# Optimization experiments

Measured on AMD Instinct MI355X. Metric: run time of the kernel, lower is better.

The kernel has to match this reference:

```python
import math
import jax, jax.numpy as jnp
import numpy as np

N = 8192; DEG = 32; E = N * DEG; H = 128
NB_NODE = 3; NB_EDGE = 4
UPPER_T = 1.0; LOWER_T = 0.01; NUM_ITERS = 1000
EPS_LN = 1e-5

def from_binary(s):
    # [..., bits] 0/1 ints -> integer code
    return (s * (2 ** jnp.arange(s.shape[-1], dtype=s.dtype))).sum(-1)

def layer_norm(x, g, b):
    mu = x.mean(-1, keepdims=True)
    v = ((x - mu) ** 2).mean(-1, keepdims=True)
    return (x - mu) / jnp.sqrt(v + EPS_LN) * g + b

def entmax15(logits):
    z = -jnp.sort(-logits, axis=-1)  # descending
    cz = jnp.cumsum(z, -1); cz2 = jnp.cumsum(z * z, -1)
    k = jnp.arange(1, logits.shape[-1] + 1, dtype=logits.dtype)
    mz = cz / k; mz2 = cz2 / k
    discr = jax.nn.relu(mz ** 2 - mz2 + 1.0 / k)
    tau_c = mz - jnp.sqrt(discr + 1e-8)
    kidx = (z > tau_c).sum(-1, keepdims=True)
    tau = jnp.take_along_axis(tau_c, kidx - 1, axis=-1)
    return jax.nn.relu(logits - tau) ** 2

def sparsemax(logits):
    z = -jnp.sort(-logits, axis=-1)
    cz = jnp.cumsum(z, -1)
    k = jnp.arange(1, logits.shape[-1] + 1, dtype=logits.dtype)
    kidx = (k * z > cz - 1.0).sum(-1, keepdims=True)
    cumk = jnp.take_along_axis(cz, kidx - 1, axis=-1)
    tau = (cumk - 1.0) / kidx.astype(logits.dtype)
    return jax.nn.relu(logits - tau)

def interpolated_probs(logits, u):
    p_soft = jax.nn.softmax(logits, -1)
    p15 = entmax15(logits)
    ps = sparsemax(logits)
    w_low = u * 2.0
    low = (1.0 - w_low) * p_soft + w_low * p15
    w_high = (u - 0.5) * 2.0
    high = (1.0 - w_high) * p15 + w_high * ps
    return jnp.where(u <= 0.5, low, high)

def setup_inputs():
    key = jax.random.key(0)
    ks = jax.random.split(key, 20)
    s = 1.0 / math.sqrt(H)
    node_states = jax.random.randint(ks[0], (N, NB_NODE), 0, 2, dtype=jnp.int32)
    edge_states = jax.random.randint(ks[1], (E, NB_EDGE), 0, 2, dtype=jnp.int32)
    scalars = jax.random.uniform(ks[2], (E, 1), jnp.float32)
    # uniform in-degree DEG, dst sorted, first edge per node is its self-loop
    dst = jnp.repeat(jnp.arange(N, dtype=jnp.int32), DEG)
    src = jax.random.randint(ks[3], (N, DEG), 0, N, dtype=jnp.int32).at[:, 0].set(jnp.arange(N, dtype=jnp.int32)).reshape(-1)
    edge_index = jnp.stack([src, dst])
    rev_idx = jax.random.permutation(ks[4], E).astype(jnp.int32)
    def w(k, shape):
        return jax.random.normal(k, shape, jnp.float32) * s
    return {
        'node_states': node_states, 'edge_states': edge_states, 'scalars': scalars,
        'edge_index': edge_index, 'rev_idx': rev_idx, 'training_step': 500,
        'emb_virtual': w(ks[5], (2 ** (NB_NODE + 1), H)),
        'emb_recv': w(ks[6], (2 ** (NB_NODE + 1), H)),
        'emb_edge': w(ks[7], (2 ** NB_EDGE, H)),
        'emb_static': w(ks[8], (4, H)),
        'Wq': w(ks[9], (H, H)), 'Wk': w(ks[10], (H, H)), 'Wv': w(ks[11], (H, H)),
        'Wek': w(ks[12], (H, H)), 'Wev': w(ks[13], (H, H)), 'Wcomb': w(ks[14], (3 * H, H)),
        'gW1': w(ks[15], (H, H)), 'gb1': jnp.zeros((H,), jnp.float32),
        'gW2': w(ks[16], (H, 1)), 'gb2': jnp.full((1,), -5.0, jnp.float32),
        'ln_q_s': jnp.ones((H,), jnp.float32), 'ln_q_b': jnp.zeros((H,), jnp.float32),
        'ln_k_s': jnp.ones((H,), jnp.float32), 'ln_k_b': jnp.zeros((H,), jnp.float32),
        'ln_ke_s': jnp.ones((H,), jnp.float32), 'ln_ke_b': jnp.zeros((H,), jnp.float32),
    }

def reference(node_states, edge_states, scalars, edge_index, rev_idx, training_step,
              emb_virtual, emb_recv, emb_edge, emb_static,
              Wq, Wk, Wv, Wek, Wev, Wcomb, gW1, gb1, gW2, gb2,
              ln_q_s, ln_q_b, ln_k_s, ln_k_b, ln_ke_s, ln_ke_b):
    src, dst = edge_index[0], edge_index[1]
    node_fts = emb_virtual[2 * from_binary(node_states)]   # [N,H] (use_select_best=False path)
    edge_fts = emb_edge[from_binary(edge_states)]           # [E,H]
    Q = layer_norm(node_fts @ Wq, ln_q_s, ln_q_b)
    Kn = layer_norm(node_fts @ Wk, ln_k_s, ln_k_b)
    Vn = node_fts @ Wv
    u = jax.nn.sigmoid(jax.nn.relu(node_fts @ gW1 + gb1) @ gW2 + gb2)  # [N,1] sparsity gate
    # ---- combined edge K/V ----
    sel = emb_recv[2 * from_binary(node_states[src])]
    # per-node scalars come from the unique self-loop edge of each node
    node_scalars = jnp.zeros((N, 1), scalars.dtype).at[dst].add(jnp.where((src == dst)[:, None], scalars, 0.0))
    sender_s, recv_s = node_scalars[src], node_scalars[dst]
    rlx = (scalars < recv_s).astype(jnp.int32)
    rlx_d = (sender_s + scalars < recv_s).astype(jnp.int32)
    static_fts = emb_static[from_binary(jnp.concatenate([rlx, rlx_d], -1))]
    combined = jnp.concatenate([edge_fts, edge_fts[rev_idx], static_fts], -1) @ Wcomb
    edge_K = layer_norm(sel @ Wek, ln_ke_s, ln_ke_b)
    edge_V = combined @ Wev
    Kc = Kn[src] + edge_K
    Vc = Vn[src] + edge_V
    # ---- to_dense_batch over destination node (dst is sorted) ----
    counts = jax.ops.segment_sum(jnp.ones(E, jnp.int32), dst, num_segments=N)
    starts = jnp.cumsum(counts) - counts
    pos = jnp.arange(E, dtype=jnp.int32) - starts[dst]
    denseK = jnp.zeros((N, DEG, H), Kc.dtype).at[dst, pos].set(Kc)
    denseV = jnp.zeros((N, DEG, H), Vc.dtype).at[dst, pos].set(Vc)
    mask = jnp.zeros((N, DEG), bool).at[dst, pos].set(True)
    cK = jnp.concatenate([Kn[:, None], denseK], 1)   # [N,1+DEG,H] self + neighbors
    cV = jnp.concatenate([Vn[:, None], denseV], 1)
    cmask = jnp.concatenate([jnp.ones((N, 1), bool), mask], 1)
    logits = jnp.einsum('nh,nkh->nk', Q, cK) / math.sqrt(H)
    logits = jnp.where(cmask, logits, -1e9)
    sparse_probs = interpolated_probs(logits, u)
    is_sel = (sparse_probs > 1e-4).astype(logits.dtype)
    hard = is_sel / (is_sel.sum(1, keepdims=True) + 1e-9)  # attention='entmax_average'
    if training_step == -1:
        attn = hard
    else:
        tau = UPPER_T * (LOWER_T / UPPER_T) ** (training_step / NUM_ITERS)  # temp anneal
        beta = min(max(tau, 0.01), 1.0)
        if beta > 0.01:
            sp = jax.nn.softmax(logits, -1) * cmask
            sp = sp / (sp.sum(1, keepdims=True) + 1e-9)
            gp = (1.0 - beta) * sparse_probs + beta * sp
        else:
            gp = sparse_probs
        attn = jax.lax.stop_gradient(hard - gp) + gp  # straight-through
    attn = attn * cmask
    agg = jnp.einsum('nk,nkh->nh', attn, cV)
    return node_fts + agg, edge_fts + agg[dst]
```

## Files before the change

kernel.cpp:

```cpp
#include <hip/hip_runtime.h>
#include <hip/hip_bf16.h>

#define NN 8192
#define EE 262144
#define HH 128
#define DEGC 32

#define WS_NF    0
#define WS_EF    1024
#define WS_VNT   3072
#define WS_AP    4096
#define WS_BP    6144
#define WS_CP    8192
#define WS_QT    8704
#define WS_KNT   9728
#define WS_EKT   10752
#define WS_U8    11776
#define WS_CN    11784
#define WS_NS    19976
#define WS_CE    28168
#define WS_COEF  290312

__global__ __launch_bounds__(128) void k_pre(
    const float* __restrict__ embV, const float* __restrict__ embR,
    const float* __restrict__ embE, const float* __restrict__ embS,
    const float* __restrict__ Wq, const float* __restrict__ Wk, const float* __restrict__ Wv,
    const float* __restrict__ Wev, const float* __restrict__ Wcomb,
    const float* __restrict__ gW1, const float* __restrict__ gb1,
    const float* __restrict__ gW2, const float* __restrict__ gb2,
    const float* __restrict__ Wek,
    const float* __restrict__ lnqs, const float* __restrict__ lnqb,
    const float* __restrict__ lnks, const float* __restrict__ lnkb,
    const float* __restrict__ lnes, const float* __restrict__ lneb,
    const int* __restrict__ node_states, const int* __restrict__ edge_states,
    const float* __restrict__ scalars, const int* __restrict__ src,
    float* __restrict__ ws)
{
  __shared__ float x[HH];
  __shared__ float y[HH];
  __shared__ float red[4];
  const int b = blockIdx.x, t = threadIdx.x;

  if (b < 24) {
    const int which = b >> 3, rr = b & 7;
    const float* xs = (which == 2 ? embR : embV) + 2*rr*HH;
    const float* W  = (which == 0 ? Wq : (which == 1 ? Wk : Wek));
    const float* ls = (which == 0 ? lnqs : (which == 1 ? lnks : lnes));
    const float* lb = (which == 0 ? lnqb : (which == 1 ? lnkb : lneb));
    float* outp = ws + (which == 0 ? WS_QT : (which == 1 ? WS_KNT : WS_EKT)) + rr*HH;
    x[t] = xs[t];
    __syncthreads();
    float acc = 0.f;
    for (int k = 0; k < HH; ++k) acc = fmaf(x[k], W[k*HH + t], acc);
    float s1 = acc;
    for (int off = 32; off; off >>= 1) s1 += __shfl_down(s1, off);
    if ((t & 63) == 0) red[t >> 6] = s1;
    __syncthreads();
    const float mu = (red[0] + red[1]) / 128.f;
    __syncthreads();
    const float dd = acc - mu;
    float s2 = dd * dd;
    for (int off = 32; off; off >>= 1) s2 += __shfl_down(s2, off);
    if ((t & 63) == 0) red[t >> 6] = s2;
    __syncthreads();
    const float var = (red[0] + red[1]) / 128.f;
    outp[t] = dd * (1.0f / sqrtf(var + 1e-5f)) * ls[t] + lb[t];
  } else if (b < 76) {
    int c, mode; const float* xs; const float* W1; float* outp = nullptr;
    if (b < 32)      { c = b-24; xs = embV + 2*c*HH; W1 = Wv;            mode = 0; outp = ws+WS_VNT+c*HH; }
    else if (b < 40) { c = b-32; xs = embV + 2*c*HH; W1 = gW1;           mode = 1; }
    else if (b < 56) { c = b-40; xs = embE + c*HH;   W1 = Wcomb;         mode = 2; outp = ws+WS_AP+c*HH; }
    else if (b < 72) { c = b-56; xs = embE + c*HH;   W1 = Wcomb+HH*HH;   mode = 2; outp = ws+WS_BP+c*HH; }
    else             { c = b-72; xs = embS + c*HH;   W1 = Wcomb+2*HH*HH; mode = 2; outp = ws+WS_CP+c*HH; }
    x[t] = xs[t];
    if (b >= 24 && b < 32) ws[WS_NF + c*HH + t] = x[t];
    if (b >= 40 && b < 56) ws[WS_EF + c*HH + t] = x[t];
    __syncthreads();
    float acc = 0.f;
    for (int k = 0; k < HH; ++k) acc = fmaf(x[k], W1[k*HH + t], acc);
    if (mode == 1) {
      acc = fmaxf(acc + gb1[t], 0.f);
      y[t] = acc;
      __syncthreads();
      if (t == 0) {
        float s = 0.f;
        for (int i = 0; i < HH; ++i) s += y[i] * gW2[i];
        s += gb2[0];
        ws[WS_U8 + c] = 1.0f / (1.0f + expf(-s));
      }
    } else if (mode == 2) {
      y[t] = acc;
      __syncthreads();
      float a2 = 0.f;
      for (int k = 0; k < HH; ++k) a2 = fmaf(y[k], Wev[k*HH + t], a2);
      outp[t] = a2;
    } else {
      outp[t] = acc;
    }
  } else if (b < 2124) {
    const int e = (b - 76)*128 + t;
    const int4 p = ((const int4*)edge_states)[e];
    ((int*)(ws + WS_CE))[e] = p.x + 2*p.y + 4*p.z + 8*p.w;
  } else {
    const int n = (b - 2124)*128 + t;
    const int* p = node_states + 3*n;
    ((int*)(ws + WS_CN))[n] = p[0] + 2*p[1] + 4*p[2];
    float s = 0.f;
    const int base = n*DEGC;
    for (int d = 0; d < DEGC; ++d)
      if (src[base + d] == n) s += scalars[base + d];
    ws[WS_NS + n] = s;
  }
}

__global__ __launch_bounds__(256) void k_attn(
    const int* __restrict__ src, const int* __restrict__ rev,
    const float* __restrict__ scalars, const float* __restrict__ wsf,
    const int* __restrict__ cn, const float* __restrict__ nsc,
    const int* __restrict__ ce, float* __restrict__ coef)
{
  const int t = threadIdx.x;
  const int l = t & 63;
  const int n = blockIdx.x*4 + (t >> 6);
  const int cn_n = cn[n];
  const float rs = nsc[n];
  const int base = n*DEGC;

  int cs = 0, m = 0, mr = 0; float scl = 0.f, ssv = 0.f;
  if (l < DEGC) {
    const int e = base + l;
    const int s = src[e];
    m   = ce[e];
    const int re = rev[e];
    mr  = ce[re];
    scl = scalars[e];
    cs  = cn[s];
    ssv = nsc[s];
  }

  const float invs = 0.08838834764831845f;
  const int j8 = l & 7, p8 = l >> 3;
  float part = 0.f;
  {
    const float* q  = wsf + WS_QT  + cn_n*HH;
    const float* kn = wsf + WS_KNT + j8*HH;
    const float* ek = wsf + WS_EKT + j8*HH;
    #pragma unroll
    for (int hh = 0; hh < 16; ++hh) {
      const int h = p8*16 + hh;
      part = fmaf(q[h], kn[h] + ek[h], part);
    }
  }
  part += __shfl_xor(part, 8);
  part += __shfl_xor(part, 16);
  part += __shfl_xor(part, 32);
  const float Dj = part * invs;
  float Drow[8];
  #pragma unroll
  for (int jj = 0; jj < 8; ++jj) Drow[jj] = __shfl(Dj, jj);
  float d0p;
  {
    const float* q  = wsf + WS_QT  + cn_n*HH;
    const float* kn = wsf + WS_KNT + cn_n*HH;
    d0p = q[l]*kn[l] + q[l+64]*kn[l+64];
  }
  #pragma unroll
  for (int off = 32; off; off >>= 1) d0p += __shfl_xor(d0p, off);
  const float z0 = d0p * invs;

  unsigned long long cpack = (l < DEGC) ? (1ull << (6*cs)) : 0ull;
  #pragma unroll
  for (int off = 32; off; off >>= 1) cpack += __shfl_xor(cpack, off);
  int cntO[8];
  #pragma unroll
  for (int jj = 0; jj < 8; ++jj) cntO[jj] = (int)((cpack >> (6*jj)) & 63);

  float gv[9]; int gc[9];
  #pragma unroll
  for (int jj = 0; jj < 8; ++jj) { gv[jj] = Drow[jj]; gc[jj] = cntO[jj]; }
  gv[8] = z0; gc[8] = 1;
  #pragma unroll
  for (int a = 0; a < 8; ++a) {
    #pragma unroll
    for (int q = 0; q < 8; ++q) {
      if (q < 8-a && gv[q] < gv[q+1]) {
        float tv = gv[q]; gv[q] = gv[q+1]; gv[q+1] = tv;
        int tcx = gc[q]; gc[q] = gc[q+1]; gc[q+1] = tcx;
      }
    }
  }

  float z = gv[8];
  {
    int rem = l; bool found = false;
    #pragma unroll
    for (int g = 0; g < 9; ++g) {
      const bool hit = !found && (rem < gc[g]);
      if (hit) { z = gv[g]; found = true; }
      if (!found) rem -= gc[g];
    }
  }
  const float kk = (float)(l + 1);
  float cz = z, cz2 = z*z;
  #pragma unroll
  for (int off = 1; off <= 32; off <<= 1) {
    const float a1 = __shfl_up(cz, off);
    const float a2 = __shfl_up(cz2, off);
    if (l >= off) { cz += a1; cz2 += a2; }
  }
  const float mz = cz/kk, mz2v = cz2/kk;
  const float dscr = fmaxf(mz*mz - mz2v + 1.0f/kk, 0.0f);
  const float tcv = mz - sqrtf(dscr + 1e-8f);
  const bool act = (l < DEGC + 1);
  const unsigned long long msk33 = (1ull << (DEGC + 1)) - 1ull;
  const unsigned long long b1 = __ballot(act && (z > tcv));
  const unsigned long long b2 = __ballot(act && (kk*z > cz - 1.0f));
  const int c15 = __popcll(b1 & msk33);
  const int csp = __popcll(b2 & msk33);
  const float tau15 = __shfl(tcv, c15 - 1);
  const float czc   = __shfl(cz,  csp - 1);
  const float tausp = (czc - 1.0f) / (float)csp;

  float mx = -1e30f;
  #pragma unroll
  for (int g = 0; g < 9; ++g) if (gc[g] > 0) mx = fmaxf(mx, gv[g]);
  float den = 0.f;
  #pragma unroll
  for (int g = 0; g < 9; ++g) den += (float)gc[g] * expf(gv[g] - mx);
  const float uu = wsf[WS_U8 + cn_n];

  auto prob = [&](float lg) -> float {
    const float psm = expf(lg - mx) / den;
    const float r15 = fmaxf(lg - tau15, 0.f);
    const float p15 = r15 * r15;
    const float psp = fmaxf(lg - tausp, 0.f);
    if (uu <= 0.5f) { const float w = 2.f*uu; return (1.f-w)*psm + w*p15; }
    const float w = 2.f*(uu - 0.5f); return (1.f-w)*p15 + w*psp;
  };

  int selmask = 0;
  #pragma unroll
  for (int jj = 0; jj < 8; ++jj) if (prob(Drow[jj]) > 1e-4f) selmask |= (1 << jj);
  const int sels = (prob(z0) > 1e-4f) ? 1 : 0;
  int cntsel = sels;
  #pragma unroll
  for (int jj = 0; jj < 8; ++jj) cntsel += ((selmask >> jj) & 1) * cntO[jj];
  const float inv = 1.0f / ((float)cntsel + 1e-9f);

  const bool sel = (l < DEGC) && (((selmask >> cs) & 1) != 0);
  unsigned long long pa0 = (sel && m < 8)   ? (1ull << (6*m))      : 0ull;
  unsigned long long pa1 = (sel && m >= 8)  ? (1ull << (6*(m-8)))  : 0ull;
  unsigned long long pb0 = (sel && mr < 8)  ? (1ull << (6*mr))     : 0ull;
  unsigned long long pb1 = (sel && mr >= 8) ? (1ull << (6*(mr-8))) : 0ull;
  unsigned int pc = 0;
  if (sel) {
    const int scode = ((scl < rs) ? 1 : 0) + (((ssv + scl) < rs) ? 2 : 0);
    pc = 1u << (6*scode);
  }
  #pragma unroll
  for (int off = 32; off; off >>= 1) {
    pa0 += __shfl_xor(pa0, off);
    pa1 += __shfl_xor(pa1, off);
    pb0 += __shfl_xor(pb0, off);
    pb1 += __shfl_xor(pb1, off);
    pc  += __shfl_xor(pc, off);
  }

  if (l < 44) {
    float w;
    if (l < 8) {
      w = ((selmask >> l) & 1) ? inv * (float)((cpack >> (6*l)) & 63) : 0.f;
      if (l == cn_n && sels) w += inv;
    } else if (l < 16) {
      w = inv * (float)((pa0 >> (6*(l-8))) & 63);
    } else if (l < 24) {
      w = inv * (float)((pa1 >> (6*(l-16))) & 63);
    } else if (l < 32) {
      w = inv * (float)((pb0 >> (6*(l-24))) & 63);
    } else if (l < 40) {
      w = inv * (float)((pb1 >> (6*(l-32))) & 63);
    } else {
      w = inv * (float)((pc >> (6*(l-40))) & 63);
    }
    coef[n*44 + l] = w;
  }
}

__global__ __launch_bounds__(256) void k_out(
    const float* __restrict__ wsf, const int* __restrict__ cn,
    const int* __restrict__ ce, const float* __restrict__ coef,
    float* __restrict__ out0, float* __restrict__ out1)
{
  __shared__ __align__(16) float tab[24*HH];
  const int t = threadIdx.x;
  const int lane = t & 63;
  for (int i = t; i < 24*HH; i += 256) tab[i] = wsf[WS_NF + i];
  float2 R[44];
  #pragma unroll
  for (int j = 0; j < 44; ++j)
    R[j] = *reinterpret_cast<const float2*>(wsf + WS_VNT + j*HH + 2*lane);
  __syncthreads();
  const float2* T = (const float2*)tab;
  const int wave = t >> 6;
  const int wg = blockIdx.x*4 + wave;
  #pragma unroll
  for (int it = 0; it < 2; ++it) {
    const int n = wg*2 + it;
    const float* cf = coef + n*44;
    float ax = 0.f, ay = 0.f;
    #pragma unroll
    for (int j = 0; j < 44; ++j) {
      const float w = cf[j];
      ax = fmaf(w, R[j].x, ax);
      ay = fmaf(w, R[j].y, ay);
    }
    const int cnn = cn[n];
    const float2 nf = T[cnn*64 + lane];
    union { float2 f; unsigned long long u; } r0;
    r0.f.x = nf.x + ax; r0.f.y = nf.y + ay;
    __builtin_nontemporal_store(r0.u,
        reinterpret_cast<unsigned long long*>(out0 + n*HH + 2*lane));
    const int ebase = n*DEGC;
    #pragma unroll
    for (int d = 0; d < DEGC; ++d) {
      const int cd = ce[ebase + d];
      const float2 ef = T[(8+cd)*64 + lane];
      union { float2 f; unsigned long long u; } r1;
      r1.f.x = ef.x + ax; r1.f.y = ef.y + ay;
      __builtin_nontemporal_store(r1.u,
          reinterpret_cast<unsigned long long*>(out1 + (ebase+d)*HH + 2*lane));
    }
  }
}

extern "C" void kernel_launch(void* const* d_in, const int* in_sizes, int n_in,
                              void* d_out, int out_size, void* d_ws, size_t ws_size,
                              hipStream_t stream)
{
  (void)in_sizes; (void)n_in; (void)out_size; (void)ws_size;
  const int*   node_states = (const int*)d_in[0];
  const int*   edge_states = (const int*)d_in[1];
  const float* scalars     = (const float*)d_in[2];
  const int*   edge_index  = (const int*)d_in[3];
  const int*   rev_idx     = (const int*)d_in[4];
  const float* embV  = (const float*)d_in[6];
  const float* embR  = (const float*)d_in[7];
  const float* embE  = (const float*)d_in[8];
  const float* embS  = (const float*)d_in[9];
  const float* Wq    = (const float*)d_in[10];
  const float* Wk    = (const float*)d_in[11];
  const float* Wv    = (const float*)d_in[12];
  const float* Wek   = (const float*)d_in[13];
  const float* Wev   = (const float*)d_in[14];
  const float* Wcomb = (const float*)d_in[15];
  const float* gW1   = (const float*)d_in[16];
  const float* gb1   = (const float*)d_in[17];
  const float* gW2   = (const float*)d_in[18];
  const float* gb2   = (const float*)d_in[19];
  const float* lnqs  = (const float*)d_in[20];
  const float* lnqb  = (const float*)d_in[21];
  const float* lnks  = (const float*)d_in[22];
  const float* lnkb  = (const float*)d_in[23];
  const float* lnes  = (const float*)d_in[24];
  const float* lneb  = (const float*)d_in[25];

  float* ws = (float*)d_ws;
  const int* src = edge_index;
  float* out0 = (float*)d_out;
  float* out1 = out0 + NN*HH;

  k_pre<<<dim3(2188), dim3(128), 0, stream>>>(embV, embR, embE, embS,
      Wq, Wk, Wv, Wev, Wcomb, gW1, gb1, gW2, gb2, Wek,
      lnqs, lnqb, lnks, lnkb, lnes, lneb,
      node_states, edge_states, scalars, src, ws);
  k_attn<<<dim3(NN/4), dim3(256), 0, stream>>>(src, rev_idx, scalars, ws,
      (const int*)(ws + WS_CN), ws + WS_NS, (const int*)(ws + WS_CE), ws + WS_COEF);
  k_out<<<dim3(1024), dim3(256), 0, stream>>>(ws, (const int*)(ws + WS_CN),
      (const int*)(ws + WS_CE), ws + WS_COEF, out0, out1);
}
```

Measured before the change: 224.3 us.

## Fuse attention-coefficient and output kernels; compute edge codes inline

Merges the attention-coefficient kernel and the output-writing kernel into one. Per-node coefficients now pass through wavefront shuffles instead of a global buffer, and edge state codes are decoded from the raw int4 inputs rather than from a precomputed workspace array. This removes a kernel launch, the coefficient and edge-code round trips through global memory, and most of k_pre's blocks. In exchange, each block reloads the 24x128 lookup table into shared memory and each lane loads 44 V vectors, once per four nodes instead of once per eight. Register pressure in the fused kernel is also higher.

```diff
diff --git a/kernel.cpp b/kernel.cpp
--- a/kernel.cpp
+++ b/kernel.cpp
@@ -18,8 +18,6 @@
 #define WS_U8    11776
 #define WS_CN    11784
 #define WS_NS    19976
-#define WS_CE    28168
-#define WS_COEF  290312
 
 __global__ __launch_bounds__(128) void k_pre(
     const float* __restrict__ embV, const float* __restrict__ embR,
@@ -32,7 +30,7 @@
     const float* __restrict__ lnqs, const float* __restrict__ lnqb,
     const float* __restrict__ lnks, const float* __restrict__ lnkb,
     const float* __restrict__ lnes, const float* __restrict__ lneb,
-    const int* __restrict__ node_states, const int* __restrict__ edge_states,
+    const int* __restrict__ node_states,
     const float* __restrict__ scalars, const int* __restrict__ src,
     float* __restrict__ ws)
 {
@@ -97,12 +95,8 @@
     } else {
       outp[t] = acc;
     }
-  } else if (b < 2124) {
-    const int e = (b - 76)*128 + t;
-    const int4 p = ((const int4*)edge_states)[e];
-    ((int*)(ws + WS_CE))[e] = p.x + 2*p.y + 4*p.z + 8*p.w;
   } else {
-    const int n = (b - 2124)*128 + t;
+    const int n = (b - 76)*128 + t;
     const int* p = node_states + 3*n;
     ((int*)(ws + WS_CN))[n] = p[0] + 2*p[1] + 4*p[2];
     float s = 0.f;
@@ -113,14 +107,19 @@
   }
 }
 
-__global__ __launch_bounds__(256) void k_attn(
+__global__ __launch_bounds__(256) void k_fused(
     const int* __restrict__ src, const int* __restrict__ rev,
-    const float* __restrict__ scalars, const float* __restrict__ wsf,
+    const float* __restrict__ scalars, const int* __restrict__ edge_states,
+    const float* __restrict__ wsf,
     const int* __restrict__ cn, const float* __restrict__ nsc,
-    const int* __restrict__ ce, float* __restrict__ coef)
+    float* __restrict__ out0, float* __restrict__ out1)
 {
+  __shared__ __align__(16) float tab[24*HH];
   const int t = threadIdx.x;
   const int l = t & 63;
+  for (int i = t; i < 24*HH; i += 256) tab[i] = wsf[WS_NF + i];
+  __syncthreads();
+
   const int n = blockIdx.x*4 + (t >> 6);
   const int cn_n = cn[n];
   const float rs = nsc[n];
@@ -130,9 +129,11 @@
   if (l < DEGC) {
     const int e = base + l;
     const int s = src[e];
-    m   = ce[e];
+    const int4 pe = ((const int4*)edge_states)[e];
+    m = pe.x + 2*pe.y + 4*pe.z + 8*pe.w;
     const int re = rev[e];
-    mr  = ce[re];
+    const int4 pr = ((const int4*)edge_states)[re];
+    mr = pr.x + 2*pr.y + 4*pr.z + 8*pr.w;
     scl = scalars[e];
     cs  = cn[s];
     ssv = nsc[s];
@@ -266,70 +267,47 @@
     pc  += __shfl_xor(pc, off);
   }
 
-  if (l < 44) {
-    float w;
-    if (l < 8) {
-      w = ((selmask >> l) & 1) ? inv * (float)((cpack >> (6*l)) & 63) : 0.f;
-      if (l == cn_n && sels) w += inv;
-    } else if (l < 16) {
-      w = inv * (float)((pa0 >> (6*(l-8))) & 63);
-    } else if (l < 24) {
-      w = inv * (float)((pa1 >> (6*(l-16))) & 63);
-    } else if (l < 32) {
-      w = inv * (float)((pb0 >> (6*(l-24))) & 63);
-    } else if (l < 40) {
-      w = inv * (float)((pb1 >> (6*(l-32))) & 63);
-    } else {
-      w = inv * (float)((pc >> (6*(l-40))) & 63);
-    }
-    coef[n*44 + l] = w;
-  }
-}
-
-__global__ __launch_bounds__(256) void k_out(
-    const float* __restrict__ wsf, const int* __restrict__ cn,
-    const int* __restrict__ ce, const float* __restrict__ coef,
-    float* __restrict__ out0, float* __restrict__ out1)
-{
-  __shared__ __align__(16) float tab[24*HH];
-  const int t = threadIdx.x;
-  const int lane = t & 63;
-  for (int i = t; i < 24*HH; i += 256) tab[i] = wsf[WS_NF + i];
+  float w = 0.f;
+  if (l < 8) {
+    w = ((selmask >> l) & 1) ? inv * (float)((cpack >> (6*l)) & 63) : 0.f;
+    if (l == cn_n && sels) w += inv;
+  } else if (l < 16) {
+    w = inv * (float)((pa0 >> (6*(l-8))) & 63);
+  } else if (l < 24) {
+    w = inv * (float)((pa1 >> (6*(l-16))) & 63);
+  } else if (l < 32) {
+    w = inv * (float)((pb0 >> (6*(l-24))) & 63);
+  } else if (l < 40) {
+    w = inv * (float)((pb1 >> (6*(l-32))) & 63);
+  } else if (l < 44) {
+    w = inv * (float)((pc >> (6*(l-40))) & 63);
+  }
+
   float2 R[44];
   #pragma unroll
   for (int j = 0; j < 44; ++j)
-    R[j] = *reinterpret_cast<const float2*>(wsf + WS_VNT + j*HH + 2*lane);
-  __syncthreads();
+    R[j] = *reinterpret_cast<const float2*>(wsf + WS_VNT + j*HH + 2*l);
+  float ax = 0.f, ay = 0.f;
+  #pragma unroll
+  for (int j = 0; j < 44; ++j) {
+    const float wj = __shfl(w, j);
+    ax = fmaf(wj, R[j].x, ax);
+    ay = fmaf(wj, R[j].y, ay);
+  }
   const float2* T = (const float2*)tab;
-  const int wave = t >> 6;
-  const int wg = blockIdx.x*4 + wave;
-  #pragma unroll
-  for (int it = 0; it < 2; ++it) {
-    const int n = wg*2 + it;
-    const float* cf = coef + n*44;
-    float ax = 0.f, ay = 0.f;
-    #pragma unroll
-    for (int j = 0; j < 44; ++j) {
-      const float w = cf[j];
-      ax = fmaf(w, R[j].x, ax);
-      ay = fmaf(w, R[j].y, ay);
-    }
-    const int cnn = cn[n];
-    const float2 nf = T[cnn*64 + lane];
-    union { float2 f; unsigned long long u; } r0;
-    r0.f.x = nf.x + ax; r0.f.y = nf.y + ay;
-    __builtin_nontemporal_store(r0.u,
-        reinterpret_cast<unsigned long long*>(out0 + n*HH + 2*lane));
-    const int ebase = n*DEGC;
-    #pragma unroll
-    for (int d = 0; d < DEGC; ++d) {
-      const int cd = ce[ebase + d];
-      const float2 ef = T[(8+cd)*64 + lane];
-      union { float2 f; unsigned long long u; } r1;
-      r1.f.x = ef.x + ax; r1.f.y = ef.y + ay;
-      __builtin_nontemporal_store(r1.u,
-          reinterpret_cast<unsigned long long*>(out1 + (ebase+d)*HH + 2*lane));
-    }
+  const float2 nf = T[cn_n*64 + l];
+  union { float2 f; unsigned long long u; } r0;
+  r0.f.x = nf.x + ax; r0.f.y = nf.y + ay;
+  __builtin_nontemporal_store(r0.u,
+      reinterpret_cast<unsigned long long*>(out0 + n*HH + 2*l));
+  #pragma unroll
+  for (int d = 0; d < DEGC; ++d) {
+    const int cd = __shfl(m, d);
+    const float2 ef = T[(8+cd)*64 + l];
+    union { float2 f; unsigned long long u; } r1;
+    r1.f.x = ef.x + ax; r1.f.y = ef.y + ay;
+    __builtin_nontemporal_store(r1.u,
+        reinterpret_cast<unsigned long long*>(out1 + (base+d)*HH + 2*l));
   }
 }
 
@@ -369,12 +347,10 @@
   float* out0 = (float*)d_out;
   float* out1 = out0 + NN*HH;
 
-  k_pre<<<dim3(2188), dim3(128), 0, stream>>>(embV, embR, embE, embS,
+  k_pre<<<dim3(140), dim3(128), 0, stream>>>(embV, embR, embE, embS,
       Wq, Wk, Wv, Wev, Wcomb, gW1, gb1, gW2, gb2, Wek,
       lnqs, lnqb, lnks, lnkb, lnes, lneb,
-      node_states, edge_states, scalars, src, ws);
-  k_attn<<<dim3(NN/4), dim3(256), 0, stream>>>(src, rev_idx, scalars, ws,
-      (const int*)(ws + WS_CN), ws + WS_NS, (const int*)(ws + WS_CE), ws + WS_COEF);
-  k_out<<<dim3(1024), dim3(256), 0, stream>>>(ws, (const int*)(ws + WS_CN),
-      (const int*)(ws + WS_CE), ws + WS_COEF, out0, out1);
+      node_states, scalars, src, ws);
+  k_fused<<<dim3(NN/4), dim3(256), 0, stream>>>(src, rev_idx, scalars, edge_states,
+      ws, (const int*)(ws + WS_CN), ws + WS_NS, out0, out1);
 }
```

Result: faster. 219.6 us (-2.1%).
